# Kernel tuning notes

Hardware: AMD Instinct MI355X
Metric: run time of the kernel (lower is better)

## Reference

```python
import jax, jax.numpy as jnp
import numpy as np
import math

D_MODEL = 1024
N_HEADS = 16
D_K = D_MODEL // N_HEADS
THRESH = 0.1  # attention probs below this are zeroed


def setup_inputs() -> dict:
    key = jax.random.key(0)
    ks = jax.random.split(key, 9)
    B, S, D = 2, 2048, D_MODEL
    scale = 1.0 / math.sqrt(D)
    x = jax.random.normal(ks[0], (B, S, D), dtype=jnp.float32)
    Wq = jax.random.normal(ks[1], (D, D), dtype=jnp.float32) * scale
    bq = jax.random.normal(ks[2], (D,), dtype=jnp.float32) * 0.01
    Wk = jax.random.normal(ks[3], (D, D), dtype=jnp.float32) * scale
    bk = jax.random.normal(ks[4], (D,), dtype=jnp.float32) * 0.01
    Wv = jax.random.normal(ks[5], (D, D), dtype=jnp.float32) * scale
    bv = jax.random.normal(ks[6], (D,), dtype=jnp.float32) * 0.01
    Wo = jax.random.normal(ks[7], (D, D), dtype=jnp.float32) * scale
    bo = jax.random.normal(ks[8], (D,), dtype=jnp.float32) * 0.01
    return {"x": x, "Wq": Wq, "bq": bq, "Wk": Wk, "bk": bk,
            "Wv": Wv, "bv": bv, "Wo": Wo, "bo": bo}


def _split_heads(t):
    B, S, D = t.shape
    return t.reshape(B, S, N_HEADS, D_K).transpose(0, 2, 1, 3)  # [B,H,S,dk]


def reference(x, Wq, bq, Wk, bk, Wv, bv, Wo, bo):
    # torch nn.Linear: y = x @ W.T + b
    q = _split_heads(x @ Wq.T + bq)
    k = _split_heads(x @ Wk.T + bk)
    v = _split_heads(x @ Wv.T + bv)
    scores = jnp.einsum('bhqd,bhkd->bhqk', q, k) / math.sqrt(D_K)
    probs = jax.nn.softmax(scores, axis=-1)          # full unmasked softmax (returned)
    keep = probs >= THRESH                            # ~low_attention_mask
    probs_model = jnp.where(keep, probs, 0.0)        # masked_fill; dropout is identity in eval
    ctx = jnp.einsum('bhqk,bhkd->bhqd', probs_model, v)
    B, H, S, dk = ctx.shape
    merged = ctx.transpose(0, 2, 1, 3).reshape(B, S, H * dk)
    out = merged @ Wo.T + bo
    attention_sum = probs.sum(axis=1)                # [B,S,S] sum over heads
    attention_mask = keep.astype(jnp.float32).sum(axis=1)  # [B,S,S]
    return (out, attention_sum, attention_mask)
```

## Files before the change

kernel.cpp:

```cpp
#include <hip/hip_runtime.h>

#define SDIM 2048
#define DDIM 1024
#define NH 16
#define DK 64
#define NB 2
#define MROWS (NB * SDIM)
#define MAXEV 65536
#define EXPC 0.18033688011112f
#define L01 -3.3219281f

typedef _Float16 f16x8 __attribute__((ext_vector_type(8)));
typedef _Float16 f16x4 __attribute__((ext_vector_type(4)));
typedef float f32x4 __attribute__((ext_vector_type(4)));

__device__ __forceinline__ void ld_lds16(const _Float16* g, _Float16* l) {
  __builtin_amdgcn_global_load_lds(
      (const __attribute__((address_space(1))) void*)g,
      (__attribute__((address_space(3))) void*)l, 16, 0, 0);
}

__global__ __launch_bounds__(256) void cvt_f16(
    const float* __restrict__ x, const float* __restrict__ wq,
    const float* __restrict__ wk, const float* __restrict__ wv,
    _Float16* __restrict__ xh, _Float16* __restrict__ wqh,
    _Float16* __restrict__ wkh, _Float16* __restrict__ wvh) {
  int i = blockIdx.x * 256 + threadIdx.x;
  const float* src;
  _Float16* dst;
  int off;
  if (i < 1048576) {
    src = x; dst = xh; off = i;
  } else if (i < 1310720) {
    src = wq; dst = wqh; off = i - 1048576;
  } else if (i < 1572864) {
    src = wk; dst = wkh; off = i - 1310720;
  } else {
    src = wv; dst = wvh; off = i - 1572864;
  }
  float4 v = ((const float4*)src)[off];
  f16x4 h;
  h[0] = (_Float16)v.x; h[1] = (_Float16)v.y;
  h[2] = (_Float16)v.z; h[3] = (_Float16)v.w;
  ((f16x4*)dst)[off] = h;
}

__global__ __launch_bounds__(256, 2) void proj_gemm(
    const _Float16* __restrict__ xh, const _Float16* __restrict__ Wqh,
    const _Float16* __restrict__ Wkh, const _Float16* __restrict__ Wvh,
    const float* __restrict__ bq, const float* __restrict__ bk,
    const float* __restrict__ bv, _Float16* __restrict__ Qo,
    _Float16* __restrict__ Ko, float* __restrict__ Vo) {
  __shared__ _Float16 sA[2][128 * 64];
  __shared__ _Float16 sB[2][128 * 64];
  const int t = threadIdx.x;
  const int lane = t & 63, wv = t >> 6;
  const int lr = lane & 15, quad = lane >> 4;
  const int wm = wv >> 1, wn = wv & 1;
  const int m0 = blockIdx.y * 128, n0 = blockIdx.x * 128;
  const int z = blockIdx.z;
  const _Float16* Bp = z == 0 ? Wqh : (z == 1 ? Wkh : Wvh);
  const float* bias = z == 0 ? bq : (z == 1 ? bk : bv);

  const int strow = t >> 3;
  const int stchunk = t & 7;
  const int stsrc = (stchunk ^ (strow & 7)) * 8;

  f32x4 acc[4][4];
#pragma unroll
  for (int i = 0; i < 4; ++i)
#pragma unroll
    for (int j = 0; j < 4; ++j) acc[i][j] = (f32x4){0.f, 0.f, 0.f, 0.f};

#define PSTAGE(K0, IB)                                                     \
  {                                                                        \
    _Pragma("unroll") for (int i = 0; i < 4; ++i) {                        \
      const int row = i * 32 + strow;                                      \
      ld_lds16(&xh[(size_t)(m0 + row) * DDIM + (K0) + stsrc],              \
               &sA[IB][row * 64 + stchunk * 8]);                           \
      ld_lds16(&Bp[(size_t)(n0 + row) * DDIM + (K0) + stsrc],              \
               &sB[IB][row * 64 + stchunk * 8]);                           \
    }                                                                      \
  }

  PSTAGE(0, 0);
  int cur = 0;
#pragma unroll 1
  for (int k0 = 0; k0 < DDIM; k0 += 64) {
    if (k0 + 64 < DDIM) PSTAGE(k0 + 64, cur ^ 1);
    asm volatile("" ::: "memory");
    if (k0 + 64 < DDIM)
      asm volatile("s_waitcnt vmcnt(8)" ::: "memory");
    else
      asm volatile("s_waitcnt vmcnt(0)" ::: "memory");
    __builtin_amdgcn_s_barrier();
    asm volatile("" ::: "memory");
    f16x8 af[4][2], bf[4][2];
#pragma unroll
    for (int i = 0; i < 4; ++i)
#pragma unroll
      for (int kk = 0; kk < 2; ++kk) {
        const int ph = ((kk * 4 + quad) ^ (lr & 7)) * 8;
        af[i][kk] = *(const f16x8*)&sA[cur][(wm * 64 + i * 16 + lr) * 64 + ph];
        bf[i][kk] = *(const f16x8*)&sB[cur][(wn * 64 + i * 16 + lr) * 64 + ph];
      }
    __builtin_amdgcn_s_setprio(1);
#pragma unroll
    for (int kk = 0; kk < 2; ++kk)
#pragma unroll
      for (int i = 0; i < 4; ++i)
#pragma unroll
        for (int j = 0; j < 4; ++j)
          acc[i][j] = __builtin_amdgcn_mfma_f32_16x16x32_f16(
              af[i][kk], bf[j][kk], acc[i][j], 0, 0, 0);
    __builtin_amdgcn_s_setprio(0);
    asm volatile("" ::: "memory");
    __builtin_amdgcn_s_barrier();
    cur ^= 1;
  }
#undef PSTAGE
#pragma unroll
  for (int j = 0; j < 4; ++j) {
    const int ng = n0 + wn * 64 + j * 16 + lr;
    const float bvv = bias[ng];
    const int h = ng >> 6, d = ng & 63;
#pragma unroll
    for (int i = 0; i < 4; ++i) {
#pragma unroll
      for (int r = 0; r < 4; ++r) {
        const int mg = m0 + wm * 64 + i * 16 + quad * 4 + r;
        const int b = mg >> 11, s = mg & 2047;
        const float o = acc[i][j][r] + bvv;
        const size_t off = ((size_t)(b * NH + h) * SDIM + s) * DK + d;
        if (z == 0)
          Qo[off] = (_Float16)(o * EXPC);
        else if (z == 1)
          Ko[off] = (_Float16)o;
        else
          Vo[off] = o;
      }
    }
  }
}

__global__ __launch_bounds__(256, 4) void attn_denom(
    const _Float16* __restrict__ Q, const _Float16* __restrict__ K,
    float* __restrict__ laOut) {
  __shared__ __align__(16) _Float16 KS[4 * 4096];
  const int t = threadIdx.x;
  const int lane = t & 63, wave = t >> 6;
  const int quad = lane >> 4, lr = lane & 15;
  const int id = blockIdx.x;
  const int xcd = id & 7, inner = id >> 3;
  const int bh = xcd * 4 + (inner >> 5);
  const int q0 = (inner & 31) * 64;
  const _Float16* Qh = Q + (size_t)bh * SDIM * DK;
  const _Float16* Kh = K + (size_t)bh * SDIM * DK;
  const size_t qoff = (size_t)(q0 + wave * 16 + lr) * DK + quad * 8;
  const f16x8 aq0 = *(const f16x8*)&Qh[qoff];
  const f16x8 aq1 = *(const f16x8*)&Qh[qoff + 32];
  const int strow = t >> 3, stchunk = t & 7;
  const int stsrc = (stchunk ^ (strow & 7)) * 8;
  const int ph0 = (quad ^ (lr & 7)) * 8;
  const int ph1 = ((4 + quad) ^ (lr & 7)) * 8;

#define STAGE_DN(KP, BUF)                                                  \
  {                                                                        \
    _Pragma("unroll") for (int i = 0; i < 2; ++i)                          \
        ld_lds16(&(KP)[(size_t)(i * 32 + strow) * DK + stsrc],             \
                 &(BUF)[(i * 32 + strow) * 64 + stchunk * 8]);             \
  }

#define COMPUTE_DN(BUF)                                                   \
  _Pragma("unroll") for (int c = 0; c < 4; ++c) {                         \
    f16x8 b0 = *(const f16x8*)&(BUF)[(c * 16 + lr) * 64 + ph0];           \
    f16x8 b1 = *(const f16x8*)&(BUF)[(c * 16 + lr) * 64 + ph1];           \
    f32x4 acc = {0.f, 0.f, 0.f, 0.f};                                     \
    acc = __builtin_amdgcn_mfma_f32_16x16x32_f16(aq0, b0, acc, 0, 0, 0);  \
    acc = __builtin_amdgcn_mfma_f32_16x16x32_f16(aq1, b1, acc, 0, 0, 0);  \
    _Pragma("unroll") for (int r = 0; r < 4; ++r)                         \
        dsum[r] += __builtin_amdgcn_exp2f(acc[r]);                        \
  }

  float dsum[4] = {0.f, 0.f, 0.f, 0.f};
  const _Float16* kp = Kh;
  STAGE_DN(kp, KS);
  kp += 64 * DK;
  STAGE_DN(kp, KS + 4096);
  kp += 64 * DK;
  int cb = 0;
#pragma unroll 1
  for (int kt = 0; kt < 32; ++kt) {
    if (kt + 2 < 32) {
      STAGE_DN(kp, KS + ((cb + 2) & 3) * 4096);
      kp += 64 * DK;
    }
    asm volatile("" ::: "memory");
    if (kt + 2 < 32)
      asm volatile("s_waitcnt vmcnt(4)" ::: "memory");
    else if (kt + 1 < 32)
      asm volatile("s_waitcnt vmcnt(2)" ::: "memory");
    else
      asm volatile("s_waitcnt vmcnt(0)" ::: "memory");
    __builtin_amdgcn_s_barrier();
    asm volatile("" ::: "memory");
    __builtin_amdgcn_s_setprio(1);
    COMPUTE_DN(KS + cb * 4096);
    __builtin_amdgcn_s_setprio(0);
    cb = (cb + 1) & 3;
  }
#pragma unroll
  for (int m = 1; m < 16; m <<= 1)
#pragma unroll
    for (int r = 0; r < 4; ++r)
      dsum[r] += __shfl_xor(dsum[r], m, 64);
  if (lr == 0) {
#pragma unroll
    for (int r = 0; r < 4; ++r)
      laOut[(size_t)bh * SDIM + q0 + wave * 16 + quad * 4 + r] =
          -__builtin_amdgcn_logf(dsum[r]);
  }
#undef STAGE_DN
#undef COMPUTE_DN
}

__global__ __launch_bounds__(256, 4) void attn_pass2(
    const _Float16* __restrict__ Q, const _Float16* __restrict__ K,
    const float* __restrict__ la, float* __restrict__ attSum,
    float* __restrict__ attMask, float4* __restrict__ ev,
    int* __restrict__ ecnt) {
  __shared__ __align__(16) _Float16 KS[4 * 4096];
  float* Tbuf = (float*)KS;
  const int t = threadIdx.x;
  const int lane = t & 63, wave = t >> 6;
  const int quad = lane >> 4, lr = lane & 15;
  const int id = blockIdx.x;
  const int xcd = id & 7, inner = id >> 3;
  const int b = xcd >> 2;
  const int q0 = (((xcd >> 1) & 1) * 16 + (inner >> 4)) * 64;
  const int k0 = ((xcd & 1) * 16 + (inner & 15)) * 64;
  const int strow = t >> 3, stchunk = t & 7;
  const int stsrc = (stchunk ^ (strow & 7)) * 8;
  const int ph0 = (quad ^ (lr & 7)) * 8;
  const int ph1 = ((4 + quad) ^ (lr & 7)) * 8;

  const size_t qbase = ((size_t)(b * NH) * SDIM + q0 + wave * 16 + lr) * DK;
  const size_t dbase = (size_t)(b * NH) * SDIM + q0 + wave * 16 + quad * 4;
  const size_t hstep = (size_t)SDIM * DK;

  float asum[4][4] = {};
  float mx01 = -1e30f, mx23 = -1e30f;

  f16x8 a0c, a1c, a0n, a1n;
  float4 lavc, lavn;

#define STAGE1(KP, BUF)                                                      \
  {                                                                          \
    _Pragma("unroll") for (int i = 0; i < 2; ++i)                            \
        ld_lds16(&(KP)[(size_t)(i * 32 + strow) * DK + stsrc],               \
                 &(BUF)[(i * 32 + strow) * 64 + stchunk * 8]);               \
  }

#define LOADQ1(QP, LAP, A0, A1, LV)                                          \
  {                                                                          \
    A0 = *(const f16x8*)&(QP)[quad * 8];                                     \
    A1 = *(const f16x8*)&(QP)[32 + quad * 8];                                \
    LV = *(const float4*)(LAP);                                              \
  }

#define COMPUTE1(BUF, A0, A1, LV)                                            \
  {                                                                          \
    const f32x4 cinit = {LV.x, LV.y, LV.z, LV.w};                            \
    _Pragma("unroll") for (int c = 0; c < 4; ++c) {                          \
      f16x8 b0 = *(const f16x8*)&(BUF)[(c * 16 + lr) * 64 + ph0];            \
      f16x8 b1 = *(const f16x8*)&(BUF)[(c * 16 + lr) * 64 + ph1];            \
      f32x4 acc = cinit;                  \
      acc = __builtin_amdgcn_mfma_f32_16x16x32_f16(A0, b0, acc, 0, 0, 0);    \
      acc = __builtin_amdgcn_mfma_f32_16x16x32_f16(A1, b1, acc, 0, 0, 0);    \
      mx01 = fmaxf(fmaxf(acc[0], acc[1]), mx01);                 \
      mx23 = fmaxf(fmaxf(acc[2], acc[3]), mx23);                             \
      asum[c][0] += __builtin_amdgcn_exp2f(acc[0]);                          \
      asum[c][1] += __builtin_amdgcn_exp2f(acc[1]);                          \
      asum[c][2] += __builtin_amdgcn_exp2f(acc[2]);                          \
      asum[c][3] += __builtin_amdgcn_exp2f(acc[3]);                          \
    }                                                                        \
  }

  const _Float16* kp = K + (size_t)(b * NH) * hstep + (size_t)k0 * DK;
  const _Float16* qp = Q + qbase;
  const float* lap = la + dbase;
  STAGE1(kp, KS);
  kp += hstep;
  STAGE1(kp, KS + 4096);
  kp += hstep;
  LOADQ1(qp, lap, a0c, a1c, lavc);
  qp += hstep; lap += SDIM;
  int cb = 0;
#pragma unroll 1
  for (int h = 0; h < NH; ++h) {
    if (h + 2 < NH) {
      STAGE1(kp, KS + ((cb + 2) & 3) * 4096);
      kp += hstep;
    }
    if (h + 1 < NH) {
      LOADQ1(qp, lap, a0n, a1n, lavn);
      qp += hstep; lap += SDIM;
    }
    asm volatile("" ::: "memory");
    if (h == NH - 1)
      asm volatile("s_waitcnt vmcnt(6)" ::: "memory");
    else
      asm volatile("s_waitcnt vmcnt(10)" ::: "memory");
    __builtin_amdgcn_s_barrier();
    asm volatile("" ::: "memory");
    __builtin_amdgcn_s_setprio(1);
    COMPUTE1(KS + cb * 4096, a0c, a1c, lavc);
    __builtin_amdgcn_s_setprio(0);
    if (h + 1 < NH) {
      a0c = a0n; a1c = a1n; lavc = lavn;
    }
    cb = (cb + 1) & 3;
  }
#undef STAGE1
#undef LOADQ1
#undef COMPUTE1

  const float mx = fmaxf(mx01, mx23);
  if (__any(mx >= L01)) {
    float amask[4][4] = {};
#pragma unroll 1
    for (int h = 0; h < NH; ++h) {
      const _Float16* Kp =
          K + (size_t)(b * NH + h) * hstep + (size_t)k0 * DK;
      const size_t ho = (size_t)h * hstep;
      const f16x8 aq0 = *(const f16x8*)&Q[qbase + ho + quad * 8];
      const f16x8 aq1 = *(const f16x8*)&Q[qbase + ho + 32 + quad * 8];
      const float4 l4 = *(const float4*)&la[dbase + (size_t)h * SDIM];
      const float lar[4] = {l4.x, l4.y, l4.z, l4.w};
#pragma unroll 1
      for (int c = 0; c < 4; ++c) {
        const f16x8 b0 = *(const f16x8*)&Kp[(c * 16 + lr) * DK + quad * 8];
        const f16x8 b1 = *(const f16x8*)&Kp[(c * 16 + lr) * DK + 32 + quad * 8];
        f32x4 acc = {0.f, 0.f, 0.f, 0.f};
        acc = __builtin_amdgcn_mfma_f32_16x16x32_f16(aq0, b0, acc, 0, 0, 0);
        acc = __builtin_amdgcn_mfma_f32_16x16x32_f16(aq1, b1, acc, 0, 0, 0);
#pragma unroll 1
        for (int r = 0; r < 4; ++r) {
          const float p = __builtin_amdgcn_exp2f(acc[r] + lar[r]);
          if (p >= 0.1f) {
            amask[c][r] += 1.0f;
            int idx = atomicAdd(ecnt, 1);
            if (idx < MAXEV)
              ev[idx] = make_float4(
                  __int_as_float(b * NH + h),
                  __int_as_float(q0 + wave * 16 + quad * 4 + r),
                  __int_as_float(k0 + c * 16 + lr), p);
          }
        }
      }
    }
#pragma unroll
    for (int c = 0; c < 4; ++c)
#pragma unroll
      for (int r = 0; r < 4; ++r)
        if (amask[c][r] != 0.0f) {
          const size_t row = (size_t)(b * SDIM) + q0 + wave * 16 + quad * 4 + r;
          attMask[row * SDIM + k0 + c * 16 + lr] = amask[c][r];
        }
  }
  const int g8 = t >> 3;
  const int l8 = (t & 7) * 4;
  __syncthreads();
#pragma unroll
  for (int c = 0; c < 4; ++c)
#pragma unroll
    for (int r = 0; r < 4; ++r)
      Tbuf[(wave * 16 + quad * 4 + r) * 68 + c * 16 + lr] = asum[c][r];
  __syncthreads();
#pragma unroll
  for (int p = 0; p < 2; ++p)
#pragma unroll
    for (int qh = 0; qh < 2; ++qh) {
      const int row = p * 32 + g8, col = qh * 32 + l8;
      f32x4 v = *(const f32x4*)&Tbuf[row * 68 + col];
      __builtin_nontemporal_store(
          v, (f32x4*)&attSum[((size_t)(b * SDIM) + q0 + row) * SDIM + k0 + col]);
    }
}

__global__ __launch_bounds__(64) void apply_events(
    const float4* __restrict__ ev, const int* __restrict__ ecnt,
    const float* __restrict__ V, float* __restrict__ merged,
    int* __restrict__ flags) {
  int n = *ecnt;
  if (n > MAXEV) n = MAXEV;
  const int d = threadIdx.x;
  for (int e = blockIdx.x; e < n; e += gridDim.x) {
    float4 r = ev[e];
    int bh = __float_as_int(r.x);
    int q = __float_as_int(r.y);
    int kc = __float_as_int(r.z);
    float p = r.w;
    int b = bh >> 4, h = bh & 15;
    atomicAdd(&merged[((size_t)(b * SDIM + q)) * DDIM + h * DK + d],
              p * V[((size_t)bh * SDIM + kc) * DK + d]);
    if (d == 0) flags[b * SDIM + q] = 1;
  }
}

__global__ __launch_bounds__(256) void out_gemm(const float* __restrict__ A,
                                                const float* __restrict__ W,
                                                const float* __restrict__ bias,
                                                float* __restrict__ out,
                                                const int* __restrict__ flags) {
  __shared__ float As[16][68];
  __shared__ float Ws[16][68];
  __shared__ int anyF;
  const int t = threadIdx.x;
  const int tx = t & 15, ty = t >> 4;
  const int m0 = blockIdx.y * 64;
  const int n0 = blockIdx.x * 64;
  if (t == 0) anyF = 0;
  __syncthreads();
  if (t < 64 && flags[m0 + t]) anyF = 1;
  __syncthreads();
  const int nb = n0 + tx * 4;
  const float4 bv = *(const float4*)&bias[nb];
  if (!anyF) {
#pragma unroll
    for (int r = 0; r < 4; ++r)
      *(float4*)&out[(size_t)(m0 + ty * 4 + r) * DDIM + nb] = bv;
    return;
  }
  const int lr = t >> 2;
  const int lc = (t & 3) * 4;
  float acc[4][4] = {};
  for (int k0 = 0; k0 < DDIM; k0 += 16) {
    __syncthreads();
    float4 av = *(const float4*)&A[(size_t)(m0 + lr) * DDIM + k0 + lc];
    float4 wv = *(const float4*)&W[(size_t)(n0 + lr) * DDIM + k0 + lc];
    As[lc + 0][lr] = av.x; As[lc + 1][lr] = av.y;
    As[lc + 2][lr] = av.z; As[lc + 3][lr] = av.w;
    Ws[lc + 0][lr] = wv.x; Ws[lc + 1][lr] = wv.y;
    Ws[lc + 2][lr] = wv.z; Ws[lc + 3][lr] = wv.w;
    __syncthreads();
#pragma unroll
    for (int kk = 0; kk < 16; ++kk) {
      float4 a4 = *(const float4*)&As[kk][ty * 4];
      float4 b4 = *(const float4*)&Ws[kk][tx * 4];
      const float a[4] = {a4.x, a4.y, a4.z, a4.w};
      const float b[4] = {b4.x, b4.y, b4.z, b4.w};
#pragma unroll
      for (int r = 0; r < 4; ++r)
#pragma unroll
        for (int c = 0; c < 4; ++c)
          acc[r][c] = fmaf(a[r], b[c], acc[r][c]);
    }
  }
#pragma unroll
  for (int r = 0; r < 4; ++r) {
    float4 o;
    o.x = acc[r][0] + bv.x;
    o.y = acc[r][1] + bv.y;
    o.z = acc[r][2] + bv.z;
    o.w = acc[r][3] + bv.w;
    *(float4*)&out[(size_t)(m0 + ty * 4 + r) * DDIM + nb] = o;
  }
}

extern "C" void kernel_launch(void* const* d_in, const int* in_sizes, int n_in,
                              void* d_out, int out_size, void* d_ws,
                              size_t ws_size, hipStream_t stream) {
  const float* x = (const float*)d_in[0];
  const float* Wq = (const float*)d_in[1];
  const float* bq = (const float*)d_in[2];
  const float* Wk = (const float*)d_in[3];
  const float* bk = (const float*)d_in[4];
  const float* Wv = (const float*)d_in[5];
  const float* bv = (const float*)d_in[6];
  const float* Wo = (const float*)d_in[7];
  const float* bo = (const float*)d_in[8];

  float* out = (float*)d_out;
  float* attSum = out + (size_t)MROWS * DDIM;
  float* attMask = attSum + (size_t)NB * SDIM * SDIM;

  char* ws = (char*)d_ws;
  const size_t bigF = (size_t)MROWS * DDIM * sizeof(float);
  const size_t bigH = (size_t)MROWS * DDIM * sizeof(_Float16);
  const size_t wH = (size_t)DDIM * DDIM * sizeof(_Float16);
  _Float16* Qh = (_Float16*)ws;  ws += bigH;
  _Float16* Kh = (_Float16*)ws;  ws += bigH;
  float* V = (float*)ws;         ws += bigF;
  float* merged = (float*)ws;    ws += bigF;
  _Float16* xh = (_Float16*)ws;  ws += bigH;
  _Float16* Wqh = (_Float16*)ws; ws += wH;
  _Float16* Wkh = (_Float16*)ws; ws += wH;
  _Float16* Wvh = (_Float16*)ws; ws += wH;
  float* laBuf = (float*)ws;     ws += (size_t)NB * NH * SDIM * sizeof(float);
  float4* ev = (float4*)ws;      ws += (size_t)MAXEV * sizeof(float4);
  int* flags = (int*)ws;         ws += (size_t)MROWS * sizeof(int);
  int* ecnt = (int*)ws;          ws += 16;

  hipMemsetAsync(merged, 0, bigF, stream);
  hipMemsetAsync(flags, 0, (size_t)MROWS * sizeof(int), stream);
  hipMemsetAsync(ecnt, 0, 16, stream);
  hipMemsetAsync(attMask, 0, (size_t)NB * SDIM * SDIM * sizeof(float), stream);

  dim3 blk(256);
  cvt_f16<<<dim3(7168), blk, 0, stream>>>(x, Wq, Wk, Wv, xh, Wqh, Wkh, Wvh);
  proj_gemm<<<dim3(8, 32, 3), blk, 0, stream>>>(xh, Wqh, Wkh, Wvh, bq, bk, bv,
                                                Qh, Kh, V);
  attn_denom<<<dim3(1024), blk, 0, stream>>>(Qh, Kh, laBuf);
  attn_pass2<<<dim3(2048), blk, 0, stream>>>(Qh, Kh, laBuf, attSum,
                                             attMask, ev, ecnt);
  apply_events<<<dim3(256), dim3(64), 0, stream>>>(ev, ecnt, V, merged, flags);
  out_gemm<<<dim3(16, 64), blk, 0, stream>>>(merged, Wo, bo, out, flags);
}
```

Before: 250.2 us.

## Drop double-buffered LDS pipeline in projection GEMM and merge zeroing memsets

Replaces the double-buffered async global-to-LDS prefetch in the QKV projection GEMM with a single-buffer load, sync, compute loop, and removes the setprio hints. This halves LDS use, which may allow more resident blocks, but loads no longer overlap MFMA compute. The workspace is also reordered so merged, flags and the event counter sit next to each other and are cleared by one memset instead of three, cutting launch overhead.

```diff
diff --git a/kernel.cpp b/kernel.cpp
--- a/kernel.cpp
+++ b/kernel.cpp
@@ -51,8 +51,8 @@
     const float* __restrict__ bq, const float* __restrict__ bk,
     const float* __restrict__ bv, _Float16* __restrict__ Qo,
     _Float16* __restrict__ Ko, float* __restrict__ Vo) {
-  __shared__ _Float16 sA[2][128 * 64];
-  __shared__ _Float16 sB[2][128 * 64];
+  __shared__ _Float16 sA[128 * 64];
+  __shared__ _Float16 sB[128 * 64];
   const int t = threadIdx.x;
   const int lane = t & 63, wv = t >> 6;
   const int lr = lane & 15, quad = lane >> 4;
@@ -72,39 +72,26 @@
 #pragma unroll
     for (int j = 0; j < 4; ++j) acc[i][j] = (f32x4){0.f, 0.f, 0.f, 0.f};
 
-#define PSTAGE(K0, IB)                                                     \
-  {                                                                        \
-    _Pragma("unroll") for (int i = 0; i < 4; ++i) {                        \
-      const int row = i * 32 + strow;                                      \
-      ld_lds16(&xh[(size_t)(m0 + row) * DDIM + (K0) + stsrc],              \
-               &sA[IB][row * 64 + stchunk * 8]);                           \
-      ld_lds16(&Bp[(size_t)(n0 + row) * DDIM + (K0) + stsrc],              \
-               &sB[IB][row * 64 + stchunk * 8]);                           \
-    }                                                                      \
-  }
-
-  PSTAGE(0, 0);
-  int cur = 0;
-#pragma unroll 1
   for (int k0 = 0; k0 < DDIM; k0 += 64) {
-    if (k0 + 64 < DDIM) PSTAGE(k0 + 64, cur ^ 1);
-    asm volatile("" ::: "memory");
-    if (k0 + 64 < DDIM)
-      asm volatile("s_waitcnt vmcnt(8)" ::: "memory");
-    else
-      asm volatile("s_waitcnt vmcnt(0)" ::: "memory");
-    __builtin_amdgcn_s_barrier();
-    asm volatile("" ::: "memory");
+    __syncthreads();
+#pragma unroll
+    for (int i = 0; i < 4; ++i) {
+      const int row = i * 32 + strow;
+      ld_lds16(&xh[(size_t)(m0 + row) * DDIM + k0 + stsrc],
+               &sA[row * 64 + stchunk * 8]);
+      ld_lds16(&Bp[(size_t)(n0 + row) * DDIM + k0 + stsrc],
+               &sB[row * 64 + stchunk * 8]);
+    }
+    __syncthreads();
     f16x8 af[4][2], bf[4][2];
 #pragma unroll
     for (int i = 0; i < 4; ++i)
 #pragma unroll
       for (int kk = 0; kk < 2; ++kk) {
         const int ph = ((kk * 4 + quad) ^ (lr & 7)) * 8;
-        af[i][kk] = *(const f16x8*)&sA[cur][(wm * 64 + i * 16 + lr) * 64 + ph];
-        bf[i][kk] = *(const f16x8*)&sB[cur][(wn * 64 + i * 16 + lr) * 64 + ph];
+        af[i][kk] = *(const f16x8*)&sA[(wm * 64 + i * 16 + lr) * 64 + ph];
+        bf[i][kk] = *(const f16x8*)&sB[(wn * 64 + i * 16 + lr) * 64 + ph];
       }
-    __builtin_amdgcn_s_setprio(1);
 #pragma unroll
     for (int kk = 0; kk < 2; ++kk)
 #pragma unroll
@@ -113,12 +100,7 @@
         for (int j = 0; j < 4; ++j)
           acc[i][j] = __builtin_amdgcn_mfma_f32_16x16x32_f16(
               af[i][kk], bf[j][kk], acc[i][j], 0, 0, 0);
-    __builtin_amdgcn_s_setprio(0);
-    asm volatile("" ::: "memory");
-    __builtin_amdgcn_s_barrier();
-    cur ^= 1;
-  }
-#undef PSTAGE
+  }
 #pragma unroll
   for (int j = 0; j < 4; ++j) {
     const int ng = n0 + wn * 64 + j * 16 + lr;
@@ -489,22 +471,21 @@
   const size_t bigF = (size_t)MROWS * DDIM * sizeof(float);
   const size_t bigH = (size_t)MROWS * DDIM * sizeof(_Float16);
   const size_t wH = (size_t)DDIM * DDIM * sizeof(_Float16);
+  float* merged = (float*)ws;    ws += bigF;
+  int* flags = (int*)ws;         ws += (size_t)MROWS * sizeof(int);
+  int* ecnt = (int*)ws;          ws += 16;
+  const size_t zeroSpan = bigF + (size_t)MROWS * sizeof(int) + 16;
   _Float16* Qh = (_Float16*)ws;  ws += bigH;
   _Float16* Kh = (_Float16*)ws;  ws += bigH;
   float* V = (float*)ws;         ws += bigF;
-  float* merged = (float*)ws;    ws += bigF;
   _Float16* xh = (_Float16*)ws;  ws += bigH;
   _Float16* Wqh = (_Float16*)ws; ws += wH;
   _Float16* Wkh = (_Float16*)ws; ws += wH;
   _Float16* Wvh = (_Float16*)ws; ws += wH;
   float* laBuf = (float*)ws;     ws += (size_t)NB * NH * SDIM * sizeof(float);
   float4* ev = (float4*)ws;      ws += (size_t)MAXEV * sizeof(float4);
-  int* flags = (int*)ws;         ws += (size_t)MROWS * sizeof(int);
-  int* ecnt = (int*)ws;          ws += 16;
-
-  hipMemsetAsync(merged, 0, bigF, stream);
-  hipMemsetAsync(flags, 0, (size_t)MROWS * sizeof(int), stream);
-  hipMemsetAsync(ecnt, 0, 16, stream);
+
+  hipMemsetAsync(merged, 0, zeroSpan, stream);
   hipMemsetAsync(attMask, 0, (size_t)NB * SDIM * SDIM * sizeof(float), stream);
 
   dim3 blk(256);
```

New measurement: 250.8 us. Within noise of the previous version (+0.2%).
